# Kernel tuning notes

Hardware: AMD Instinct MI355X
Metric: run time of the kernel (lower is better)

The kernel has to match this reference:

```python
import jax, jax.numpy as jnp
import numpy as np

N = 50000
E = 800000
IN_C, HID, OUT_C = 128, 128, 40
EPS = 1e-5  # BatchNorm eps


def setup_inputs() -> dict:
    key = jax.random.key(0)
    ks = jax.random.split(key, 8)
    x = jax.random.normal(ks[0], (N, IN_C), dtype=jnp.float32)
    edge_index = jax.random.randint(ks[1], (2, E), 0, N, dtype=jnp.int64)
    s1 = 1.0 / np.sqrt(IN_C)
    s2 = 1.0 / np.sqrt(HID)
    return {
        "x": x,
        "edge_index": edge_index,
        "W1": jax.random.uniform(ks[2], (IN_C, HID), jnp.float32, -s1, s1),
        "b1": jnp.zeros((HID,), jnp.float32),
        "g1": jnp.ones((HID,), jnp.float32),
        "beta1": jnp.zeros((HID,), jnp.float32),
        "W2": jax.random.uniform(ks[3], (HID, HID), jnp.float32, -s2, s2),
        "b2": jnp.zeros((HID,), jnp.float32),
        "g2": jnp.ones((HID,), jnp.float32),
        "beta2": jnp.zeros((HID,), jnp.float32),
        "W3": jax.random.uniform(ks[4], (HID, OUT_C), jnp.float32, -s2, s2),
        "b3": jnp.zeros((OUT_C,), jnp.float32),
    }


def _gcn_norm(src, dst, num_nodes):
    # symmetric normalization D^-1/2 A D^-1/2, no self loops, unit edge weights
    deg = jax.ops.segment_sum(jnp.ones_like(dst, dtype=jnp.float32), dst,
                              num_segments=num_nodes)
    dinv = jnp.where(deg > 0, jax.lax.rsqrt(jnp.maximum(deg, 1.0)), 0.0)
    return dinv[src] * dinv[dst]  # [E]


def _conv(h, W, b, src, dst, norm, num_nodes):
    h = h @ W  # linear transform first (fewer message features)
    msg = norm[:, None] * h[src]  # [E, F] gather
    out = jax.ops.segment_sum(msg, dst, num_segments=num_nodes)  # scatter-add
    return out + b


def _bn_relu(h, g, beta):
    mu = jnp.mean(h, axis=0)
    var = jnp.mean(jnp.square(h - mu), axis=0)  # biased, as torch BN
    hn = (h - mu) * jax.lax.rsqrt(var + EPS) * g + beta
    return jax.nn.relu(hn)


def reference(x, edge_index, W1, b1, g1, beta1, W2, b2, g2, beta2, W3, b3):
    src, dst = edge_index[0], edge_index[1]
    norm = _gcn_norm(src, dst, N)  # cached=True: shared across layers
    h = _bn_relu(_conv(x, W1, b1, src, dst, norm, N), g1, beta1)
    h = _bn_relu(_conv(h, W2, b2, src, dst, norm, N), g2, beta2)
    return _conv(h, W3, b3, src, dst, norm, N)
```

## Files before the change

kernel.cpp:

```cpp
#include <hip/hip_runtime.h>
#include <hip/hip_fp16.h>

typedef _Float16 half8 __attribute__((ext_vector_type(8)));
typedef float floatx4 __attribute__((ext_vector_type(4)));


__device__ __forceinline__ void unpack8(uint4 v, float* f) {
    const __half2* hp = (const __half2*)&v;
    float2 a = __half22float2(hp[0]);
    float2 b = __half22float2(hp[1]);
    float2 c = __half22float2(hp[2]);
    float2 d = __half22float2(hp[3]);
    f[0] = a.x; f[1] = a.y; f[2] = b.x; f[3] = b.y;
    f[4] = c.x; f[5] = c.y; f[6] = d.x; f[7] = d.y;
}

__device__ __forceinline__ uint4 pack8(const float* f) {
    __half2 h0 = __floats2half2_rn(f[0], f[1]);
    __half2 h1 = __floats2half2_rn(f[2], f[3]);
    __half2 h2 = __floats2half2_rn(f[4], f[5]);
    __half2 h3 = __floats2half2_rn(f[6], f[7]);
    uint4 v;
    v.x = *(const unsigned int*)&h0;
    v.y = *(const unsigned int*)&h1;
    v.z = *(const unsigned int*)&h2;
    v.w = *(const unsigned int*)&h3;
    return v;
}

__global__ void k_zeroz(int* p, int n) {
    int i = blockIdx.x * 256 + threadIdx.x;
    if (i < n) p[i] = 0;
}


__global__ void k_packW3(const float* __restrict__ W1, const float* __restrict__ W2,
                         const float* __restrict__ W3, __half* __restrict__ Wt1,
                         __half* __restrict__ Wt2, __half* __restrict__ Wt3) {
    int i = blockIdx.x * 256 + threadIdx.x;
    if (i < 128 * 128) {
        int n = i >> 7, k = i & 127;
        Wt1[i] = __float2half(W1[(size_t)k * 128 + n]);
    } else if (i < 2 * 128 * 128) {
        int j = i - 128 * 128;
        int n = j >> 7, k = j & 127;
        Wt2[j] = __float2half(W2[(size_t)k * 128 + n]);
    } else if (i < 2 * 128 * 128 + 48 * 128) {
        int j = i - 2 * 128 * 128;
        int n = j >> 7, k = j & 127;
        Wt3[j] = (n < 40) ? __float2half(W3[(size_t)k * 40 + n]) : __half(0.f);
    }
}


__global__ void k_deg_xcd(const int* __restrict__ dst, int* __restrict__ deg,
                          int E, int rs) {
    int lo = (blockIdx.x & 7) * rs;
    int i = (blockIdx.x >> 3) * 256 + threadIdx.x;
    if (i < E) {
        int d = dst[i];
        if (d >= lo && d < lo + rs) atomicAdd(&deg[d], 1);
    }
}

__global__ void k_place_xcd(const int* __restrict__ src, const int* __restrict__ dst,
                            int* __restrict__ cursor, int* __restrict__ sidx,
                            int E, int rs) {
    int lo = (blockIdx.x & 7) * rs;
    int i = (blockIdx.x >> 3) * 256 + threadIdx.x;
    if (i < E) {
        int d = dst[i];
        if (d >= lo && d < lo + rs) {
            int pos = atomicAdd(&cursor[d], 1);
            sidx[pos] = src[i];
        }
    }
}

__global__ __launch_bounds__(256) void k_chunkscan(const int* __restrict__ deg,
                                                   int* __restrict__ bsum, int n) {
    __shared__ int ls[256];
    int t = threadIdx.x;
    int s = 0;
    int base = t * 256;
    for (int k = 0; k < 256; ++k) {
        int idx = base + k;
        if (idx < n) s += deg[idx];
    }
    ls[t] = s;
    __syncthreads();
    for (int off = 1; off < 256; off <<= 1) {
        int v = t >= off ? ls[t - off] : 0;
        __syncthreads();
        ls[t] += v;
        __syncthreads();
    }
    bsum[t] = ls[t] - s;
}

__global__ void k_scanchunk(const int* __restrict__ cnt, const int* __restrict__ bsum,
                            int* __restrict__ row_ptr, int* __restrict__ cursor,
                            float* __restrict__ dinv, int n, int E) {
    __shared__ int ls[256];
    int i = blockIdx.x * 256 + threadIdx.x;
    int v = i < n ? cnt[i] : 0;
    ls[threadIdx.x] = v;
    __syncthreads();
    for (int off = 1; off < 256; off <<= 1) {
        int t = threadIdx.x >= off ? ls[threadIdx.x - off] : 0;
        __syncthreads();
        ls[threadIdx.x] += t;
        __syncthreads();
    }
    if (i < n) {
        int ex = ls[threadIdx.x] - v + bsum[blockIdx.x];
        row_ptr[i] = ex;
        cursor[i] = ex;
        dinv[i] = v > 0 ? rsqrtf((float)v) : 0.f;
    }
    if (i == n - 1) row_ptr[n] = E;
}


template <int CT, int STRIDE, int VALID, int AMODE>
__global__ __launch_bounds__(256) void k_gemm_mfma(const void* __restrict__ Ap,
                                                   const __half* __restrict__ Wt,
                                                   const float* __restrict__ sums32,
                                                   const float* __restrict__ sumsq32,
                                                   const float* __restrict__ g,
                                                   const float* __restrict__ beta,
                                                   const float* __restrict__ dinv,
                                                   __half* __restrict__ C, int nrows) {
    __shared__ char lw[CT * 16 * 256];
    __shared__ float lsc[128], lsh[128];
    const int nu4 = CT * 16 * 16;
    for (int i = threadIdx.x; i < nu4; i += 256) {
        int row = i >> 4, k8 = i & 15;
        uint4 v = ((const uint4*)Wt)[i];
        *(uint4*)(lw + ((row * 256 + k8 * 16) ^ ((row & 7) << 4))) = v;
    }
    if (AMODE == 1 && threadIdx.x < 128) {
        int c = threadIdx.x;
        float s = 0.f, q = 0.f;
        for (int k2 = 0; k2 < 32; ++k2) {
            s += sums32[k2 * 128 + c];
            q += sumsq32[k2 * 128 + c];
        }
        float inv_n = 1.f / (float)nrows;
        float mu = s * inv_n;
        float var = q * inv_n - mu * mu;
        float rs = rsqrtf(var + 1e-5f);
        float sc = rs * g[c];
        lsc[c] = sc;
        lsh[c] = beta[c] - mu * sc;
    }
    __syncthreads();

    const int lane = threadIdx.x & 63;
    const int wid = threadIdx.x >> 6;
    const int l15 = lane & 15;
    const int lg = lane >> 4;
    const int rowbase = blockIdx.x * 128 + wid * 32;

    floatx4 acc[2][CT];
#pragma unroll
    for (int r = 0; r < 2; ++r)
#pragma unroll
        for (int c = 0; c < CT; ++c) acc[r][c] = (floatx4){0.f, 0.f, 0.f, 0.f};

    for (int kk = 0; kk < 4; ++kk) {
        half8 afrag[2];
        const int c0 = kk * 32 + lg * 8;
#pragma unroll
        for (int r = 0; r < 2; ++r) {
            int row = rowbase + r * 16 + l15;
            half8 h = {0, 0, 0, 0, 0, 0, 0, 0};
            if (row < nrows) {
                if (AMODE == 0) {
                    const float* a = (const float*)Ap + (size_t)row * 128 + c0;
                    float4 v0 = *(const float4*)a;
                    float4 v1 = *(const float4*)(a + 4);
                    h[0] = (_Float16)v0.x; h[1] = (_Float16)v0.y;
                    h[2] = (_Float16)v0.z; h[3] = (_Float16)v0.w;
                    h[4] = (_Float16)v1.x; h[5] = (_Float16)v1.y;
                    h[6] = (_Float16)v1.z; h[7] = (_Float16)v1.w;
                } else {
                    uint4 raw = *(const uint4*)((const __half*)Ap + (size_t)row * 128 + c0);
                    float f[8];
                    unpack8(raw, f);
                    float4 s0 = *(const float4*)&lsc[c0];
                    float4 s1 = *(const float4*)&lsc[c0 + 4];
                    float4 t0 = *(const float4*)&lsh[c0];
                    float4 t1 = *(const float4*)&lsh[c0 + 4];
                    h[0] = (_Float16)fmaxf(f[0] * s0.x + t0.x, 0.f);
                    h[1] = (_Float16)fmaxf(f[1] * s0.y + t0.y, 0.f);
                    h[2] = (_Float16)fmaxf(f[2] * s0.z + t0.z, 0.f);
                    h[3] = (_Float16)fmaxf(f[3] * s0.w + t0.w, 0.f);
                    h[4] = (_Float16)fmaxf(f[4] * s1.x + t1.x, 0.f);
                    h[5] = (_Float16)fmaxf(f[5] * s1.y + t1.y, 0.f);
                    h[6] = (_Float16)fmaxf(f[6] * s1.z + t1.z, 0.f);
                    h[7] = (_Float16)fmaxf(f[7] * s1.w + t1.w, 0.f);
                }
            }
            afrag[r] = h;
        }
#pragma unroll
        for (int c = 0; c < CT; ++c) {
            int wrow = c * 16 + l15;
            half8 bfrag = *(const half8*)(lw + ((wrow * 256 + kk * 64 + lg * 16) ^ ((wrow & 7) << 4)));
#pragma unroll
            for (int r = 0; r < 2; ++r)
                acc[r][c] = __builtin_amdgcn_mfma_f32_16x16x32_f16(afrag[r], bfrag, acc[r][c], 0, 0, 0);
        }
    }

#pragma unroll
    for (int r = 0; r < 2; ++r) {
        int rbase = rowbase + r * 16 + lg * 4;
        float d4[4];
#pragma unroll
        for (int j = 0; j < 4; ++j)
            d4[j] = (rbase + j) < nrows ? dinv[rbase + j] : 0.f;
#pragma unroll
        for (int c = 0; c < CT; ++c) {
            int col = c * 16 + l15;
            if (VALID != CT * 16 && col >= VALID) continue;
#pragma unroll
            for (int j = 0; j < 4; ++j) {
                int row = rbase + j;
                if (row < nrows)
                    C[(size_t)row * STRIDE + col] = __float2half(acc[r][c][j] * d4[j]);
            }
        }
    }
}


__global__ __launch_bounds__(256) void k_agg128_stats(const __half* __restrict__ M,
                                                      const int* __restrict__ rp,
                                                      const int* __restrict__ sidx,
                                                      const float* __restrict__ dinv,
                                                      __half* __restrict__ Hout,
                                                      float* __restrict__ sums32,
                                                      float* __restrict__ sumsq32, int n) {
    int d = blockIdx.x * 16 + (threadIdx.x >> 4);
    int lane = threadIdx.x & 15;
    float acc[8] = {0.f, 0.f, 0.f, 0.f, 0.f, 0.f, 0.f, 0.f};
    if (d < n) {
        int beg = rp[d], end = rp[d + 1];
        int j = beg;
        for (; j + 4 <= end; j += 4) {
            int s0 = sidx[j], s1 = sidx[j + 1], s2 = sidx[j + 2], s3 = sidx[j + 3];
            uint4 v0 = *(const uint4*)(M + (size_t)s0 * 128 + lane * 8);
            uint4 v1 = *(const uint4*)(M + (size_t)s1 * 128 + lane * 8);
            uint4 v2 = *(const uint4*)(M + (size_t)s2 * 128 + lane * 8);
            uint4 v3 = *(const uint4*)(M + (size_t)s3 * 128 + lane * 8);
            float f0[8], f1[8], f2[8], f3[8];
            unpack8(v0, f0); unpack8(v1, f1); unpack8(v2, f2); unpack8(v3, f3);
#pragma unroll
            for (int i = 0; i < 8; ++i)
                acc[i] += (f0[i] + f1[i]) + (f2[i] + f3[i]);
        }
        for (; j < end; ++j) {
            int s = sidx[j];
            uint4 v = *(const uint4*)(M + (size_t)s * 128 + lane * 8);
            float f[8];
            unpack8(v, f);
#pragma unroll
            for (int i = 0; i < 8; ++i) acc[i] += f[i];
        }
        float sc = dinv[d];
#pragma unroll
        for (int i = 0; i < 8; ++i) acc[i] *= sc;
        *(uint4*)(Hout + (size_t)d * 128 + lane * 8) = pack8(acc);
    }
    float sq[8];
#pragma unroll
    for (int i = 0; i < 8; ++i) sq[i] = acc[i] * acc[i];
#pragma unroll
    for (int m = 16; m <= 32; m <<= 1) {
#pragma unroll
        for (int i = 0; i < 8; ++i) {
            acc[i] += __shfl_xor(acc[i], m);
            sq[i]  += __shfl_xor(sq[i], m);
        }
    }
    __shared__ float lsw[2][4][16][8];
    int wid = threadIdx.x >> 6, wl = threadIdx.x & 63;
    if (wl < 16) {
#pragma unroll
        for (int i = 0; i < 8; ++i) {
            lsw[0][wid][wl][i] = acc[i];
            lsw[1][wid][wl][i] = sq[i];
        }
    }
    __syncthreads();
    if (threadIdx.x < 128) {
        int c = threadIdx.x;
        int lc = c >> 3, e = c & 7;
        float ss = 0.f, qq = 0.f;
#pragma unroll
        for (int w = 0; w < 4; ++w) {
            ss += lsw[0][w][lc][e];
            qq += lsw[1][w][lc][e];
        }
        int sh = (blockIdx.x & 31) * 128;
        atomicAdd(&sums32[sh + c], ss);
        atomicAdd(&sumsq32[sh + c], qq);
    }
}


__global__ void k_agg40_f16(const __half* __restrict__ M,
                            const int* __restrict__ rp,
                            const int* __restrict__ sidx,
                            const float* __restrict__ dinv,
                            const float* __restrict__ b3,
                            float* __restrict__ out, int n) {
    int i = blockIdx.x * 256 + threadIdx.x;
    if (i >= n * 5) return;
    int d = i / 5, q = i % 5;
    int beg = rp[d], end = rp[d + 1];
    float acc[8] = {0.f, 0.f, 0.f, 0.f, 0.f, 0.f, 0.f, 0.f};
    int j = beg;
    for (; j + 4 <= end; j += 4) {
        int s0 = sidx[j], s1 = sidx[j + 1], s2 = sidx[j + 2], s3 = sidx[j + 3];
        uint4 v0 = *(const uint4*)(M + (size_t)s0 * 64 + q * 8);
        uint4 v1 = *(const uint4*)(M + (size_t)s1 * 64 + q * 8);
        uint4 v2 = *(const uint4*)(M + (size_t)s2 * 64 + q * 8);
        uint4 v3 = *(const uint4*)(M + (size_t)s3 * 64 + q * 8);
        float f0[8], f1[8], f2[8], f3[8];
        unpack8(v0, f0); unpack8(v1, f1); unpack8(v2, f2); unpack8(v3, f3);
#pragma unroll
        for (int k = 0; k < 8; ++k)
            acc[k] += (f0[k] + f1[k]) + (f2[k] + f3[k]);
    }
    for (; j < end; ++j) {
        int s = sidx[j];
        uint4 v = *(const uint4*)(M + (size_t)s * 64 + q * 8);
        float f[8];
        unpack8(v, f);
#pragma unroll
        for (int k = 0; k < 8; ++k) acc[k] += f[k];
    }
    float sc = dinv[d];
    float4 b0 = *(const float4*)&b3[q * 8];
    float4 b1 = *(const float4*)&b3[q * 8 + 4];
    float4 r0, r1;
    r0.x = acc[0] * sc + b0.x; r0.y = acc[1] * sc + b0.y;
    r0.z = acc[2] * sc + b0.z; r0.w = acc[3] * sc + b0.w;
    r1.x = acc[4] * sc + b1.x; r1.y = acc[5] * sc + b1.y;
    r1.z = acc[6] * sc + b1.z; r1.w = acc[7] * sc + b1.w;
    float* o = out + (size_t)d * 40 + q * 8;
    *(float4*)o = r0;
    *(float4*)(o + 4) = r1;
}


extern "C" void kernel_launch(void* const* d_in, const int* in_sizes, int n_in,
                              void* d_out, int out_size, void* d_ws, size_t ws_size,
                              hipStream_t stream) {
    const float* x  = (const float*)d_in[0];
    const int*   ei = (const int*)d_in[1];
    const float* W1 = (const float*)d_in[2];
    const float* g1 = (const float*)d_in[4];
    const float* be1= (const float*)d_in[5];
    const float* W2 = (const float*)d_in[6];
    const float* g2 = (const float*)d_in[8];
    const float* be2= (const float*)d_in[9];
    const float* W3 = (const float*)d_in[10];
    const float* b3 = (const float*)d_in[11];

    const int N = in_sizes[0] / 128;
    const int E = in_sizes[1] / 2;
    const int* srcv = ei;
    const int* dstv = ei + E;
    const int NB = (N + 255) / 256;
    const int RS = (N + 7) / 8;
    const int EB8 = 8 * ((E + 255) / 256);

    __half* M    = (__half*)d_ws;
    __half* Hb   = M + (size_t)N * 128;
    __half* t3   = Hb + (size_t)N * 128;
    __half* Wt1  = t3 + (size_t)N * 64;
    __half* Wt2  = Wt1 + 128 * 128;
    __half* Wt3  = Wt2 + 128 * 128;
    float* dinv    = (float*)(Wt3 + 48 * 128);
    int*   deg     = (int*)(dinv + N);
    float* sumsA   = (float*)(deg + N);
    float* sumsqA  = sumsA + 32 * 128;
    float* sumsB   = sumsqA + 32 * 128;
    float* sumsqB  = sumsB + 32 * 128;
    int*   row_ptr = (int*)(sumsqB + 32 * 128);
    int*   cursor  = row_ptr + N + 1;
    int*   sidx    = cursor + N;
    int*   bsum    = sidx + E;
    float* out     = (float*)d_out;

    const int GB = (N + 127) / 128;
    const int ZN = N + 4 * 32 * 128;

    k_packW3<<<(2 * 128 * 128 + 48 * 128 + 255) / 256, 256, 0, stream>>>(W1, W2, W3, Wt1, Wt2, Wt3);
    k_zeroz<<<(ZN + 255) / 256, 256, 0, stream>>>(deg, ZN);
    k_deg_xcd<<<EB8, 256, 0, stream>>>(dstv, deg, E, RS);
    k_chunkscan<<<1, 256, 0, stream>>>(deg, bsum, N);
    k_scanchunk<<<NB, 256, 0, stream>>>(deg, bsum, row_ptr, cursor, dinv, N, E);
    k_place_xcd<<<EB8, 256, 0, stream>>>(srcv, dstv, cursor, sidx, E, RS);

    k_gemm_mfma<8, 128, 128, 0><<<GB, 256, 0, stream>>>(x, Wt1, nullptr, nullptr, nullptr, nullptr, dinv, M, N);
    k_agg128_stats<<<(N + 15) / 16, 256, 0, stream>>>(M, row_ptr, sidx, dinv, Hb, sumsA, sumsqA, N);

    k_gemm_mfma<8, 128, 128, 1><<<GB, 256, 0, stream>>>(Hb, Wt2, sumsA, sumsqA, g1, be1, dinv, M, N);
    k_agg128_stats<<<(N + 15) / 16, 256, 0, stream>>>(M, row_ptr, sidx, dinv, Hb, sumsB, sumsqB, N);

    k_gemm_mfma<3, 64, 40, 1><<<GB, 256, 0, stream>>>(Hb, Wt3, sumsB, sumsqB, g2, be2, dinv, t3, N);
    k_agg40_f16<<<(N * 5 + 255) / 256, 256, 0, stream>>>(t3, row_ptr, sidx, dinv, b3, out, N);
}
```

Measured before the change: 241.0 us.

## Use 16-bit edge indices and split GEMM columns with LDS-staged coalesced stores

Source indices in the CSR adjacency are stored as unsigned short instead of int, which halves the index traffic in the placement and aggregation kernels. This relies on N being below 65536. The 128-wide GEMMs now run as two column halves per row tile, doubling the block count. Each block stages its fp16 output tile in swizzled LDS and writes it back as full 16-byte row segments instead of scattered 2-byte stores. All A fragments are preloaded before the MFMA loop, at the cost of reading A twice across the column blocks and extra register pressure.

```diff
diff --git a/kernel.cpp b/kernel.cpp
--- a/kernel.cpp
+++ b/kernel.cpp
@@ -64,7 +64,7 @@
 }
 
 __global__ void k_place_xcd(const int* __restrict__ src, const int* __restrict__ dst,
-                            int* __restrict__ cursor, int* __restrict__ sidx,
+                            int* __restrict__ cursor, unsigned short* __restrict__ sidx,
                             int E, int rs) {
     int lo = (blockIdx.x & 7) * rs;
     int i = (blockIdx.x >> 3) * 256 + threadIdx.x;
@@ -72,7 +72,7 @@
         int d = dst[i];
         if (d >= lo && d < lo + rs) {
             int pos = atomicAdd(&cursor[d], 1);
-            sidx[pos] = src[i];
+            sidx[pos] = (unsigned short)src[i];
         }
     }
 }
@@ -122,7 +122,7 @@
 }
 
 
-template <int CT, int STRIDE, int VALID, int AMODE>
+template <int CT, int STRIDE, int VALID, int AMODE, int CSPLIT>
 __global__ __launch_bounds__(256) void k_gemm_mfma(const void* __restrict__ Ap,
                                                    const __half* __restrict__ Wt,
                                                    const float* __restrict__ sums32,
@@ -133,10 +133,13 @@
                                                    __half* __restrict__ C, int nrows) {
     __shared__ char lw[CT * 16 * 256];
     __shared__ float lsc[128], lsh[128];
+    const int rowblk = (CSPLIT == 2) ? (blockIdx.x >> 1) : blockIdx.x;
+    const int colblk = (CSPLIT == 2) ? (blockIdx.x & 1) : 0;
+
     const int nu4 = CT * 16 * 16;
     for (int i = threadIdx.x; i < nu4; i += 256) {
         int row = i >> 4, k8 = i & 15;
-        uint4 v = ((const uint4*)Wt)[i];
+        uint4 v = ((const uint4*)Wt)[(colblk * CT * 16 + row) * 16 + k8];
         *(uint4*)(lw + ((row * 256 + k8 * 16) ^ ((row & 7) << 4))) = v;
     }
     if (AMODE == 1 && threadIdx.x < 128) {
@@ -160,22 +163,18 @@
     const int wid = threadIdx.x >> 6;
     const int l15 = lane & 15;
     const int lg = lane >> 4;
-    const int rowbase = blockIdx.x * 128 + wid * 32;
-
-    floatx4 acc[2][CT];
-#pragma unroll
-    for (int r = 0; r < 2; ++r)
-#pragma unroll
-        for (int c = 0; c < CT; ++c) acc[r][c] = (floatx4){0.f, 0.f, 0.f, 0.f};
-
-    for (int kk = 0; kk < 4; ++kk) {
-        half8 afrag[2];
-        const int c0 = kk * 32 + lg * 8;
-#pragma unroll
-        for (int r = 0; r < 2; ++r) {
-            int row = rowbase + r * 16 + l15;
+    const int rowbase = rowblk * 128 + wid * 32;
+
+    half8 a2[2][4];
+#pragma unroll
+    for (int r = 0; r < 2; ++r) {
+        int row = rowbase + r * 16 + l15;
+        bool ok = row < nrows;
+#pragma unroll
+        for (int kk = 0; kk < 4; ++kk) {
+            const int c0 = kk * 32 + lg * 8;
             half8 h = {0, 0, 0, 0, 0, 0, 0, 0};
-            if (row < nrows) {
+            if (ok) {
                 if (AMODE == 0) {
                     const float* a = (const float*)Ap + (size_t)row * 128 + c0;
                     float4 v0 = *(const float4*)a;
@@ -202,34 +201,79 @@
                     h[7] = (_Float16)fmaxf(f[7] * s1.w + t1.w, 0.f);
                 }
             }
-            afrag[r] = h;
-        }
+            a2[r][kk] = h;
+        }
+    }
+
+    floatx4 acc[2][CT];
+#pragma unroll
+    for (int r = 0; r < 2; ++r)
+#pragma unroll
+        for (int c = 0; c < CT; ++c) acc[r][c] = (floatx4){0.f, 0.f, 0.f, 0.f};
+
+#pragma unroll
+    for (int kk = 0; kk < 4; ++kk) {
 #pragma unroll
         for (int c = 0; c < CT; ++c) {
             int wrow = c * 16 + l15;
             half8 bfrag = *(const half8*)(lw + ((wrow * 256 + kk * 64 + lg * 16) ^ ((wrow & 7) << 4)));
 #pragma unroll
             for (int r = 0; r < 2; ++r)
-                acc[r][c] = __builtin_amdgcn_mfma_f32_16x16x32_f16(afrag[r], bfrag, acc[r][c], 0, 0, 0);
-        }
-    }
-
-#pragma unroll
-    for (int r = 0; r < 2; ++r) {
-        int rbase = rowbase + r * 16 + lg * 4;
-        float d4[4];
-#pragma unroll
-        for (int j = 0; j < 4; ++j)
-            d4[j] = (rbase + j) < nrows ? dinv[rbase + j] : 0.f;
-#pragma unroll
-        for (int c = 0; c < CT; ++c) {
-            int col = c * 16 + l15;
-            if (VALID != CT * 16 && col >= VALID) continue;
+                acc[r][c] = __builtin_amdgcn_mfma_f32_16x16x32_f16(a2[r][kk], bfrag, acc[r][c], 0, 0, 0);
+        }
+    }
+
+    if (CSPLIT == 2) {
+        __syncthreads();
+        __half* ct = (__half*)lw;
+#pragma unroll
+        for (int r = 0; r < 2; ++r) {
+            int lr0 = wid * 32 + r * 16 + lg * 4;
+            float d4[4];
 #pragma unroll
             for (int j = 0; j < 4; ++j) {
-                int row = rbase + j;
-                if (row < nrows)
-                    C[(size_t)row * STRIDE + col] = __float2half(acc[r][c][j] * d4[j]);
+                int row = rowblk * 128 + lr0 + j;
+                d4[j] = row < nrows ? dinv[row] : 0.f;
+            }
+#pragma unroll
+            for (int c = 0; c < CT; ++c) {
+                int col = c * 16 + l15;
+#pragma unroll
+                for (int j = 0; j < 4; ++j) {
+                    int lrow = lr0 + j;
+                    int cc = col ^ (((lrow >> 2) & 1) << 5);
+                    ct[lrow * 64 + cc] = __float2half(acc[r][c][j] * d4[j]);
+                }
+            }
+        }
+        __syncthreads();
+        for (int i = threadIdx.x; i < 128 * 8; i += 256) {
+            int lrow = i >> 3, u = i & 7;
+            int row = rowblk * 128 + lrow;
+            if (row < nrows) {
+                int cc = (u * 8) ^ (((lrow >> 2) & 1) << 5);
+                uint4 v = *(const uint4*)&ct[lrow * 64 + cc];
+                *(uint4*)(&C[(size_t)row * STRIDE + colblk * 64 + u * 8]) = v;
+            }
+        }
+    } else {
+#pragma unroll
+        for (int r = 0; r < 2; ++r) {
+            int rbase = rowbase + r * 16 + lg * 4;
+            float d4[4];
+#pragma unroll
+            for (int j = 0; j < 4; ++j)
+                d4[j] = (rbase + j) < nrows ? dinv[rbase + j] : 0.f;
+#pragma unroll
+            for (int c = 0; c < CT; ++c) {
+                int col = c * 16 + l15;
+                if (VALID != CT * 16 && col >= VALID) continue;
+#pragma unroll
+                for (int j = 0; j < 4; ++j) {
+                    int row = rbase + j;
+                    if (row < nrows)
+                        C[(size_t)row * STRIDE + col] = __float2half(acc[r][c][j] * d4[j]);
+                }
             }
         }
     }
@@ -238,7 +282,7 @@
 
 __global__ __launch_bounds__(256) void k_agg128_stats(const __half* __restrict__ M,
                                                       const int* __restrict__ rp,
-                                                      const int* __restrict__ sidx,
+                                                      const unsigned short* __restrict__ sidx,
                                                       const float* __restrict__ dinv,
                                                       __half* __restrict__ Hout,
                                                       float* __restrict__ sums32,
@@ -313,7 +357,7 @@
 
 __global__ void k_agg40_f16(const __half* __restrict__ M,
                             const int* __restrict__ rp,
-                            const int* __restrict__ sidx,
+                            const unsigned short* __restrict__ sidx,
                             const float* __restrict__ dinv,
                             const float* __restrict__ b3,
                             float* __restrict__ out, int n) {
@@ -393,8 +437,8 @@
     float* sumsqB  = sumsB + 32 * 128;
     int*   row_ptr = (int*)(sumsqB + 32 * 128);
     int*   cursor  = row_ptr + N + 1;
-    int*   sidx    = cursor + N;
-    int*   bsum    = sidx + E;
+    unsigned short* sidx = (unsigned short*)(cursor + N);
+    int*   bsum    = (int*)(sidx + E);
     float* out     = (float*)d_out;
 
     const int GB = (N + 127) / 128;
@@ -407,12 +451,12 @@
     k_scanchunk<<<NB, 256, 0, stream>>>(deg, bsum, row_ptr, cursor, dinv, N, E);
     k_place_xcd<<<EB8, 256, 0, stream>>>(srcv, dstv, cursor, sidx, E, RS);
 
-    k_gemm_mfma<8, 128, 128, 0><<<GB, 256, 0, stream>>>(x, Wt1, nullptr, nullptr, nullptr, nullptr, dinv, M, N);
+    k_gemm_mfma<4, 128, 128, 0, 2><<<GB * 2, 256, 0, stream>>>(x, Wt1, nullptr, nullptr, nullptr, nullptr, dinv, M, N);
     k_agg128_stats<<<(N + 15) / 16, 256, 0, stream>>>(M, row_ptr, sidx, dinv, Hb, sumsA, sumsqA, N);
 
-    k_gemm_mfma<8, 128, 128, 1><<<GB, 256, 0, stream>>>(Hb, Wt2, sumsA, sumsqA, g1, be1, dinv, M, N);
+    k_gemm_mfma<4, 128, 128, 1, 2><<<GB * 2, 256, 0, stream>>>(Hb, Wt2, sumsA, sumsqA, g1, be1, dinv, M, N);
     k_agg128_stats<<<(N + 15) / 16, 256, 0, stream>>>(M, row_ptr, sidx, dinv, Hb, sumsB, sumsqB, N);
 
-    k_gemm_mfma<3, 64, 40, 1><<<GB, 256, 0, stream>>>(Hb, Wt3, sumsB, sumsqB, g2, be2, dinv, t3, N);
+    k_gemm_mfma<3, 64, 40, 1, 1><<<GB, 256, 0, stream>>>(Hb, Wt3, sumsB, sumsqB, g2, be2, dinv, t3, N);
     k_agg40_f16<<<(N * 5 + 255) / 256, 256, 0, stream>>>(t3, row_ptr, sidx, dinv, b3, out, N);
 }
```

Measured after the change: 228.2 us. 5.3% less time.
